# Performance work log

Measured on AMD Instinct MI355X. Metric: run time of the kernel, lower is better.

## Reference

```python
import jax, jax.numpy as jnp
import numpy as np

B, L, W, K, G = 8, 2048, 1024, 5, 2
OFFSET_SCALE = 2.0
EPS = 1e-5


def setup_inputs() -> dict:
    key = jax.random.key(0)
    ks = jax.random.split(key, 6)
    x = jax.random.normal(ks[0], (B, L, W), jnp.float32)
    # True = padded position
    lengths = jax.random.randint(ks[1], (B,), L // 2, L + 1)
    mask = jnp.arange(L)[None, :] >= lengths[:, None]
    # offset predictor (pointwise): one fractional offset per kernel tap
    w_off = jax.random.normal(ks[2], (W, K), jnp.float32) * 0.02
    b_off = jnp.zeros((K,), jnp.float32)
    # grouped conv weights: [groups, out_per_group, in_per_group, K]
    conv_w = jax.random.normal(ks[3], (G, W // G, W // G, K), jnp.float32) * 0.02
    conv_b = jnp.zeros((W,), jnp.float32)
    gamma = jnp.ones((W,), jnp.float32)
    beta = jnp.zeros((W,), jnp.float32)
    proj_w = jax.random.normal(ks[4], (W,), jnp.float32) * 0.02
    proj_b = jnp.zeros((), jnp.float32)
    return dict(x=x, mask=mask, w_off=w_off, b_off=b_off, conv_w=conv_w,
                conv_b=conv_b, gamma=gamma, beta=beta, proj_w=proj_w, proj_b=proj_b)


def _deform_conv1d(x, w_off, b_off, conv_w, conv_b):
    # x: [B, L, W]; returns [B, L, W]
    Bb, Ll, Ww = x.shape
    Gg, Co, Ci, Kk = conv_w.shape
    # per-position, per-tap fractional offsets in [-offset_scale, offset_scale]
    offsets = jnp.tanh(x @ w_off + b_off) * OFFSET_SCALE            # [B, L, K]
    taps = jnp.arange(Kk, dtype=x.dtype) - (Kk - 1) / 2.0           # centered taps
    pos = jnp.arange(Ll, dtype=x.dtype)[None, :, None] + taps[None, None, :] + offsets  # [B,L,K]
    p0 = jnp.floor(pos)
    frac = pos - p0                                                  # [B, L, K]
    p0i = p0.astype(jnp.int32)
    bidx = jnp.arange(Bb)[:, None, None]

    def gather(idx):
        valid = (idx >= 0) & (idx < Ll)                              # zero padding outside
        samp = x[bidx, jnp.clip(idx, 0, Ll - 1)]                     # [B, L, K, W]
        return samp * valid[..., None].astype(x.dtype)

    # linear interpolation between floor and floor+1 samples
    samp = gather(p0i) * (1.0 - frac)[..., None] + gather(p0i + 1) * frac[..., None]
    samp = samp.reshape(Bb, Ll, Kk, Gg, Ci)                          # split channels into groups
    out = jnp.einsum('blkgc,gock->blgo', samp, conv_w).reshape(Bb, Ll, Gg * Co)
    return out + conv_b


def reference(x, mask, w_off, b_off, conv_w, conv_b, gamma, beta, proj_w, proj_b):
    h = _deform_conv1d(x, w_off, b_off, conv_w, conv_b)              # [B, L, W]
    # LayerNorm over width
    mu = jnp.mean(h, axis=-1, keepdims=True)
    var = jnp.mean((h - mu) ** 2, axis=-1, keepdims=True)
    h = (h - mu) * jax.lax.rsqrt(var + EPS) * gamma + beta
    # dropout is identity in eval mode
    h = jnp.where(mask[..., None], 0.0, h)                           # masked fill
    lengths = jnp.maximum(jnp.sum(~mask, axis=1, keepdims=True).astype(h.dtype), 1.0)
    pooled = jnp.sum(h, axis=1) / lengths                            # [B, W]
    return pooled @ proj_w + proj_b                                  # [B]
```

## Files before the change

### kernel.cpp

```cpp
#include <hip/hip_runtime.h>
#include <hip/hip_bf16.h>

constexpr int Bb = 8, Ll = 2048, Ww = 1024;
constexpr int BL = Bb * Ll;

typedef short bf16x8 __attribute__((ext_vector_type(8)));
typedef float f32x4  __attribute__((ext_vector_type(4)));

__device__ inline unsigned short f2bf(float f) {
    union { float f; unsigned u; } v; v.f = f;
    unsigned u = v.u;
    unsigned r = (u + 0x7fffu + ((u >> 16) & 1u)) >> 16;
    return (unsigned short)r;
}
__device__ inline float bf2f(unsigned short h) {
    union { unsigned u; float f; } v; v.u = ((unsigned)h) << 16;
    return v.f;
}
__device__ inline unsigned lerp_pair(unsigned pa, unsigned pb, float w0, float w1) {
    union { unsigned u; float f; } alo, ahi, blo, bhi;
    alo.u = pa << 16;  ahi.u = pa & 0xffff0000u;
    blo.u = pb << 16;  bhi.u = pb & 0xffff0000u;
    float hlo = w0 * alo.f + w1 * blo.f;
    float hhi = w0 * ahi.f + w1 * bhi.f;
    union { __hip_bfloat162 h2; unsigned u; } r;
    r.h2 = __float22bfloat162_rn(float2{hlo, hhi});
    return r.u;
}

__device__ inline void gl_lds16(const unsigned short* g, unsigned short* l) {
    __builtin_amdgcn_global_load_lds(
        (const __attribute__((address_space(1))) unsigned int*)g,
        (__attribute__((address_space(3))) unsigned int*)l, 16, 0, 0);
}

__global__ void maskA_kernel(const void* __restrict__ mraw, int* __restrict__ flags) {
    const unsigned char* mb = (const unsigned char*)mraw;
    const unsigned* mw = (const unsigned*)mraw;
    int gid = blockIdx.x * 256 + threadIdx.x;
    int nonint = 0, notf = 0, hasf = 0;
    for (int i = gid; i < BL; i += 4096) { if ((i & 3) && mb[i]) nonint = 1; }
    for (int i = gid; i < BL / 4; i += 4096) {
        unsigned w = mw[i];
        if (w == 0x3f800000u) hasf = 1; else if (w) notf = 1;
    }
    if (__builtin_amdgcn_readfirstlane(__ballot(nonint) ? 1 : 0)) { if ((threadIdx.x & 63) == 0 && __ballot(nonint)) atomicOr(&flags[0], 1); }
    if ((threadIdx.x & 63) == 0) {
    }
    if (nonint) atomicOr(&flags[0], 1);
    if (notf)   atomicOr(&flags[1], 1);
    if (hasf)   atomicOr(&flags[2], 1);
}
__global__ void maskB_kernel(const void* __restrict__ mraw, const int* __restrict__ flags,
                             float* __restrict__ maskf) {
    const unsigned char* mb = (const unsigned char*)mraw;
    const unsigned* mw = (const unsigned*)mraw;
    int gid = blockIdx.x * 256 + threadIdx.x;
    int is_f32  = (!flags[1]) && flags[2];
    int is_bool = (!is_f32) && flags[0];
    for (int i = gid; i < BL; i += 4096) {
        int masked = is_bool ? (mb[i] != 0) : (mw[i] != 0u);
        maskf[i] = masked ? 0.0f : 1.0f;
    }
}

__global__ void wconv_kernel(const float* __restrict__ conv_w, unsigned short* __restrict__ w_t) {
    int gnt = blockIdx.x >> 2;
    int part = blockIdx.x & 3;
    int g = gnt / 20, nt = gnt % 20;
    int k = nt >> 2, o0 = (nt & 3) * 128;
    int tid = threadIdx.x;
    #pragma unroll
    for (int it = 0; it < 8; it++) {
        int chunk = part * 2048 + it * 256 + tid;
        int r = chunk >> 6;
        int cq = chunk & 63;
        int cs = cq >> 2, q = cq & 3;
        int o = o0 + r;
        int c0 = cs * 32 + q * 8;
        const float* src = conv_w + (((size_t)(g * 512 + o) * 512 + c0) * 5 + k);
        ushort4 lo, hi;
        lo.x = f2bf(src[0]);  lo.y = f2bf(src[5]);  lo.z = f2bf(src[10]); lo.w = f2bf(src[15]);
        hi.x = f2bf(src[20]); hi.y = f2bf(src[25]); hi.z = f2bf(src[30]); hi.w = f2bf(src[35]);
        int dst16 = (gnt * 16 + cs) * 512 + r * 4 + (q ^ (r & 3));
        *(ushort4*)&w_t[(size_t)dst16 * 8]     = lo;
        *(ushort4*)&w_t[(size_t)dst16 * 8 + 4] = hi;
    }
}

__global__ __launch_bounds__(256) void offsets_kernel(
    const float* __restrict__ x, const float* __restrict__ w_off, const float* __restrict__ b_off,
    unsigned short* __restrict__ x_bf, float4* __restrict__ pk)
{
    const int wave = threadIdx.x >> 6, lane = threadIdx.x & 63;
    const int bl = blockIdx.x * 4 + wave;
    const int l = bl & (Ll - 1);
    const int c0 = lane * 16;

    const float* xr = x + (size_t)bl * Ww + c0;
    float4 v0 = *(const float4*)(xr + 0);
    float4 v1 = *(const float4*)(xr + 4);
    float4 v2 = *(const float4*)(xr + 8);
    float4 v3 = *(const float4*)(xr + 12);
    float xv[16] = { v0.x,v0.y,v0.z,v0.w, v1.x,v1.y,v1.z,v1.w,
                     v2.x,v2.y,v2.z,v2.w, v3.x,v3.y,v3.z,v3.w };

    uint4 pa, pb;
    unsigned* pu = (unsigned*)&pa;
    #pragma unroll
    for (int j = 0; j < 4; j++) pu[j] = (unsigned)f2bf(xv[j*2]) | ((unsigned)f2bf(xv[j*2+1]) << 16);
    pu = (unsigned*)&pb;
    #pragma unroll
    for (int j = 0; j < 4; j++) pu[j] = (unsigned)f2bf(xv[8+j*2]) | ((unsigned)f2bf(xv[8+j*2+1]) << 16);
    *(uint4*)&x_bf[(size_t)bl * Ww + c0]     = pa;
    *(uint4*)&x_bf[(size_t)bl * Ww + c0 + 8] = pb;

    float acc[5] = {0.f, 0.f, 0.f, 0.f, 0.f};
    const float* wp = w_off + (size_t)c0 * 5;
    #pragma unroll
    for (int j = 0; j < 16; j++) {
        #pragma unroll
        for (int k = 0; k < 5; k++) acc[k] += xv[j] * wp[j * 5 + k];
    }
    #pragma unroll
    for (int k = 0; k < 5; k++)
        #pragma unroll
        for (int off = 32; off; off >>= 1) acc[k] += __shfl_xor(acc[k], off);

    if (lane < 5) {
        float s = (lane == 0) ? acc[0] : (lane == 1) ? acc[1] : (lane == 2) ? acc[2]
                : (lane == 3) ? acc[3] : acc[4];
        s += b_off[lane];
        float offv = tanhf(s) * 2.0f;
        float pos = (float)l + (float)(lane - 2) + offv;
        float p0 = floorf(pos);
        float frac = pos - p0;
        int i0 = (int)p0;
        int i1 = i0 + 1;
        int ok0 = (i0 >= 0) && (i0 < Ll);
        int ok1 = (i1 >= 0) && (i1 < Ll);
        float4 pkv;
        pkv.x = __int_as_float(min(max(i0, 0), Ll - 1));
        pkv.y = __int_as_float(min(max(i1, 0), Ll - 1));
        pkv.z = ok0 ? (1.0f - frac) : 0.0f;
        pkv.w = ok1 ? frac : 0.0f;
        pk[bl * 5 + lane] = pkv;
    }
}

__global__ __launch_bounds__(256, 2) void gemm_kernel(
    const unsigned short* __restrict__ x_bf, const unsigned short* __restrict__ w_t,
    const float4* __restrict__ pk, const float* __restrict__ conv_b,
    unsigned short* __restrict__ h)
{
    __shared__ unsigned short Bs[2][2 * 4096];
    const int tid = threadIdx.x;
    const int mt = blockIdx.x;
    const int nhalf = blockIdx.y;
    const int g = blockIdx.z;
    const int b = mt >> 4;
    const int lane = tid & 63, wave = tid >> 6;
    const int wr = (wave >> 1) * 64;
    const int imgsel = wave & 1;
    const int l15 = lane & 15, l4 = lane >> 4;
    const int sw = (l4 ^ (l15 & 3)) * 8;

    {
        const int nt0 = nhalf * 2;
        const unsigned short* W0 = w_t + ((size_t)((g * 20 + nt0) * 16 + 0)) * 4096;
        const unsigned short* W1 = w_t + ((size_t)((g * 20 + nt0 + 1) * 16 + 0)) * 4096;
        gl_lds16(W0 + tid * 8,        &Bs[0][tid * 8]);
        gl_lds16(W0 + 2048 + tid * 8, &Bs[0][2048 + tid * 8]);
        gl_lds16(W1 + tid * 8,        &Bs[0][4096 + tid * 8]);
        gl_lds16(W1 + 2048 + tid * 8, &Bs[0][4096 + 2048 + tid * 8]);
    }
    __syncthreads();

    f32x4 acc[4][8];
    #pragma unroll
    for (int i = 0; i < 4; i++)
        #pragma unroll
        for (int j = 0; j < 8; j++) acc[i][j] = (f32x4){0.f, 0.f, 0.f, 0.f};

    int buf = 0;
    for (int k = 0; k < 5; ++k) {
        unsigned off0[4], off1[4];
        float w0r[4], w1r[4];
        #pragma unroll
        for (int i = 0; i < 4; i++) {
            const int bl = mt * 128 + wr + i * 16 + l15;
            float4 pkv = pk[bl * 5 + k];
            const int i0 = __float_as_int(pkv.x), i1 = __float_as_int(pkv.y);
            off0[i] = (unsigned)(((b << 11) + i0) * Ww + g * 512);
            off1[i] = (unsigned)(((b << 11) + i1) * Ww + g * 512);
            w0r[i] = pkv.z; w1r[i] = pkv.w;
        }
        for (int cs = 0; cs < 16; ++cs) {
            const int it = k * 16 + cs;
            if (it < 79) {
                const int it2 = it + 1;
                const int k2 = it2 >> 4, cs2 = it2 & 15;
                const int nt0 = k2 * 4 + nhalf * 2;
                const unsigned short* W0 = w_t + ((size_t)((g * 20 + nt0) * 16 + cs2)) * 4096;
                const unsigned short* W1 = w_t + ((size_t)((g * 20 + nt0 + 1) * 16 + cs2)) * 4096;
                gl_lds16(W0 + tid * 8,        &Bs[buf ^ 1][tid * 8]);
                gl_lds16(W0 + 2048 + tid * 8, &Bs[buf ^ 1][2048 + tid * 8]);
                gl_lds16(W1 + tid * 8,        &Bs[buf ^ 1][4096 + tid * 8]);
                gl_lds16(W1 + 2048 + tid * 8, &Bs[buf ^ 1][4096 + 2048 + tid * 8]);
            }
            const int ch0 = cs * 32 + l4 * 8;
            bf16x8 af[4];
            #pragma unroll
            for (int i = 0; i < 4; i++) {
                const uint4 ua = *(const uint4*)(x_bf + off0[i] + ch0);
                const uint4 ub = *(const uint4*)(x_bf + off1[i] + ch0);
                union { unsigned u[4]; bf16x8 v; } fa;
                fa.u[0] = lerp_pair(ua.x, ub.x, w0r[i], w1r[i]);
                fa.u[1] = lerp_pair(ua.y, ub.y, w0r[i], w1r[i]);
                fa.u[2] = lerp_pair(ua.z, ub.z, w0r[i], w1r[i]);
                fa.u[3] = lerp_pair(ua.w, ub.w, w0r[i], w1r[i]);
                af[i] = fa.v;
            }
            bf16x8 bfr[8];
            #pragma unroll
            for (int j = 0; j < 8; j++)
                bfr[j] = *(const bf16x8*)&Bs[buf][imgsel * 4096 + (j * 16 + l15) * 32 + sw];
            #pragma unroll
            for (int i = 0; i < 4; i++)
                #pragma unroll
                for (int j = 0; j < 8; j++)
                    acc[i][j] = __builtin_amdgcn_mfma_f32_16x16x32_bf16(af[i], bfr[j], acc[i][j], 0, 0, 0);
            __syncthreads();
            buf ^= 1;
        }
    }
    #pragma unroll
    for (int j = 0; j < 8; j++) {
        const int col = g * 512 + nhalf * 256 + imgsel * 128 + j * 16 + l15;
        const float bias = conv_b[col];
        #pragma unroll
        for (int i = 0; i < 4; i++) {
            const int row0 = mt * 128 + wr + i * 16 + l4 * 4;
            #pragma unroll
            for (int rr = 0; rr < 4; rr++)
                h[(size_t)(row0 + rr) * Ww + col] = f2bf(acc[i][j][rr] + bias);
        }
    }
}

__global__ __launch_bounds__(256) void lnpool_kernel(
    const unsigned short* __restrict__ h, const float* __restrict__ gamma,
    const float* __restrict__ maskf, float* __restrict__ pooled)
{
    const int tid = threadIdx.x;
    const int wave = tid >> 6, lane = tid & 63;
    const int c0 = lane * 16;
    const int bl0 = blockIdx.x * 16 + wave * 4;
    const int b = bl0 >> 11;

    float g16[16];
    #pragma unroll
    for (int j = 0; j < 4; j++) {
        float4 gv = *(const float4*)(gamma + c0 + j * 4);
        g16[j*4+0] = gv.x; g16[j*4+1] = gv.y; g16[j*4+2] = gv.z; g16[j*4+3] = gv.w;
    }
    float pacc[16];
    #pragma unroll
    for (int j = 0; j < 16; j++) pacc[j] = 0.f;

    #pragma unroll
    for (int r = 0; r < 4; r++) {
        const int bl = bl0 + r;
        const float m = maskf[bl];
        const uint4 ha = *(const uint4*)(h + (size_t)bl * Ww + c0);
        const uint4 hb = *(const uint4*)(h + (size_t)bl * Ww + c0 + 8);
        float hf[16];
        const unsigned* pw = (const unsigned*)&ha;
        #pragma unroll
        for (int j = 0; j < 4; j++) {
            union { unsigned u; float f; } lo, hi;
            lo.u = pw[j] << 16; hi.u = pw[j] & 0xffff0000u;
            hf[j*2] = lo.f; hf[j*2+1] = hi.f;
        }
        pw = (const unsigned*)&hb;
        #pragma unroll
        for (int j = 0; j < 4; j++) {
            union { unsigned u; float f; } lo, hi;
            lo.u = pw[j] << 16; hi.u = pw[j] & 0xffff0000u;
            hf[8+j*2] = lo.f; hf[8+j*2+1] = hi.f;
        }
        float s1 = 0.f, s2 = 0.f;
        #pragma unroll
        for (int j = 0; j < 16; j++) { s1 += hf[j]; s2 += hf[j] * hf[j]; }
        #pragma unroll
        for (int off = 32; off; off >>= 1) {
            s1 += __shfl_xor(s1, off);
            s2 += __shfl_xor(s2, off);
        }
        const float mu = s1 * (1.0f / 1024.0f);
        const float var = s2 * (1.0f / 1024.0f) - mu * mu;
        const float rstd = rsqrtf(var + 1e-5f) * m;
        #pragma unroll
        for (int j = 0; j < 16; j++) pacc[j] += (hf[j] - mu) * rstd * g16[j];
    }
    __shared__ float spool[4][1024];
    #pragma unroll
    for (int j = 0; j < 4; j++)
        *(float4*)&spool[wave][c0 + j * 4] = *(float4*)&pacc[j * 4];
    __syncthreads();
    const int ch = tid * 4;
    float4 a = *(float4*)&spool[0][ch];
    float4 bq = *(float4*)&spool[1][ch];
    float4 cq = *(float4*)&spool[2][ch];
    float4 dq = *(float4*)&spool[3][ch];
    atomicAdd(&pooled[b * Ww + ch + 0], a.x + bq.x + cq.x + dq.x);
    atomicAdd(&pooled[b * Ww + ch + 1], a.y + bq.y + cq.y + dq.y);
    atomicAdd(&pooled[b * Ww + ch + 2], a.z + bq.z + cq.z + dq.z);
    atomicAdd(&pooled[b * Ww + ch + 3], a.w + bq.w + cq.w + dq.w);
}

__global__ void final_kernel(const float* __restrict__ pooled, const float* __restrict__ maskf,
                             const float* __restrict__ beta, const float* __restrict__ proj_w,
                             const float* __restrict__ proj_b, float* __restrict__ out)
{
    int b = blockIdx.x;
    int tid = threadIdx.x;
    float len = 0.f, dotP = 0.f, dotB = 0.f;
    for (int l = tid; l < Ll; l += 256) len += maskf[b * Ll + l];
    for (int c = tid; c < Ww; c += 256) {
        dotP += pooled[b * Ww + c] * proj_w[c];
        dotB += beta[c] * proj_w[c];
    }
    for (int off = 32; off; off >>= 1) {
        len += __shfl_down(len, off);
        dotP += __shfl_down(dotP, off);
        dotB += __shfl_down(dotB, off);
    }
    __shared__ float rl[4], rp[4], rb[4];
    int wave = tid >> 6, lane = tid & 63;
    if (lane == 0) { rl[wave] = len; rp[wave] = dotP; rb[wave] = dotB; }
    __syncthreads();
    if (tid == 0) {
        float Lt = rl[0] + rl[1] + rl[2] + rl[3];
        float Pt = rp[0] + rp[1] + rp[2] + rp[3];
        float Bt = rb[0] + rb[1] + rb[2] + rb[3];
        out[b] = Pt / fmaxf(Lt, 1.0f) + Bt + proj_b[0];
    }
}


extern "C" void kernel_launch(void* const* d_in, const int* in_sizes, int n_in,
                              void* d_out, int out_size, void* d_ws, size_t ws_size,
                              hipStream_t stream)
{
    const float* x      = (const float*)d_in[0];
    const void*  mask   = d_in[1];
    const float* w_off  = (const float*)d_in[2];
    const float* b_off  = (const float*)d_in[3];
    const float* conv_w = (const float*)d_in[4];
    const float* conv_b = (const float*)d_in[5];
    const float* gamma  = (const float*)d_in[6];
    const float* beta   = (const float*)d_in[7];
    const float* proj_w = (const float*)d_in[8];
    const float* proj_b = (const float*)d_in[9];
    float* out = (float*)d_out;

    char* ws = (char*)d_ws;
    float* maskf         = (float*)(ws + 0);
    float* pooled        = (float*)(ws + 65536);
    int*   flags         = (int*)(ws + 98304);
    float4* pk           = (float4*)(ws + 98320);
    unsigned short* w_t  = (unsigned short*)(ws + 1409040);
    unsigned short* x_bf = (unsigned short*)(ws + 6651920);
    unsigned short* h    = (unsigned short*)(ws + 40206352);

    hipMemsetAsync(pooled, 0, Bb * Ww * sizeof(float), stream);
    hipMemsetAsync(flags, 0, 16, stream);
    maskA_kernel<<<16, 256, 0, stream>>>(mask, flags);
    maskB_kernel<<<16, 256, 0, stream>>>(mask, flags, maskf);
    wconv_kernel<<<160, 256, 0, stream>>>(conv_w, w_t);
    offsets_kernel<<<BL / 4, 256, 0, stream>>>(x, w_off, b_off, x_bf, pk);
    gemm_kernel<<<dim3(128, 2, 2), 256, 0, stream>>>(x_bf, w_t, pk, conv_b, h);
    lnpool_kernel<<<1024, 256, 0, stream>>>(h, gamma, maskf, pooled);
    final_kernel<<<8, 256, 0, stream>>>(pooled, maskf, beta, proj_w, proj_b, out);
}
```

Before: 352.2 us.

## Stage interpolated A tile in shared memory and coalesce weight conversion

The GEMM now builds the interpolated A tile once per block into a double-buffered shared-memory array, alongside the weight prefetch. Before, each wave regathered and lerped its own rows from global memory, so rows were duplicated across the two waves sharing them. The weight conversion kernel is restructured so each thread reads 40 contiguous floats with vector loads and writes all five taps, replacing strided scalar reads. The change adds 16 KB of LDS per block and puts gather latency on the prefetch path, which could affect occupancy.

```diff
diff --git a/kernel.cpp b/kernel.cpp
--- a/kernel.cpp
+++ b/kernel.cpp
@@ -12,10 +12,6 @@
     unsigned u = v.u;
     unsigned r = (u + 0x7fffu + ((u >> 16) & 1u)) >> 16;
     return (unsigned short)r;
-}
-__device__ inline float bf2f(unsigned short h) {
-    union { unsigned u; float f; } v; v.u = ((unsigned)h) << 16;
-    return v.f;
 }
 __device__ inline unsigned lerp_pair(unsigned pa, unsigned pb, float w0, float w1) {
     union { unsigned u; float f; } alo, ahi, blo, bhi;
@@ -43,9 +39,6 @@
     for (int i = gid; i < BL / 4; i += 4096) {
         unsigned w = mw[i];
         if (w == 0x3f800000u) hasf = 1; else if (w) notf = 1;
-    }
-    if (__builtin_amdgcn_readfirstlane(__ballot(nonint) ? 1 : 0)) { if ((threadIdx.x & 63) == 0 && __ballot(nonint)) atomicOr(&flags[0], 1); }
-    if ((threadIdx.x & 63) == 0) {
     }
     if (nonint) atomicOr(&flags[0], 1);
     if (notf)   atomicOr(&flags[1], 1);
@@ -64,25 +57,26 @@
     }
 }
 
-__global__ void wconv_kernel(const float* __restrict__ conv_w, unsigned short* __restrict__ w_t) {
-    int gnt = blockIdx.x >> 2;
-    int part = blockIdx.x & 3;
-    int g = gnt / 20, nt = gnt % 20;
-    int k = nt >> 2, o0 = (nt & 3) * 128;
-    int tid = threadIdx.x;
-    #pragma unroll
-    for (int it = 0; it < 8; it++) {
-        int chunk = part * 2048 + it * 256 + tid;
-        int r = chunk >> 6;
-        int cq = chunk & 63;
-        int cs = cq >> 2, q = cq & 3;
-        int o = o0 + r;
-        int c0 = cs * 32 + q * 8;
-        const float* src = conv_w + (((size_t)(g * 512 + o) * 512 + c0) * 5 + k);
+__global__ __launch_bounds__(256) void wconv_kernel(const float* __restrict__ conv_w,
+                                                    unsigned short* __restrict__ w_t) {
+    int t = blockIdx.x * 256 + threadIdx.x;
+    int oct = t & 63;
+    int o   = (t >> 6) & 511;
+    int g   = t >> 15;
+    const float* src = conv_w + ((size_t)(g * 512 + o) * 512 + oct * 8) * 5;
+    float f[40];
+    #pragma unroll
+    for (int j = 0; j < 10; j++) *(float4*)&f[j * 4] = *(const float4*)&src[j * 4];
+    int r = o & 127, ob = o >> 7, cs = oct >> 2, q = oct & 3;
+    int base16 = ((g * 20 + ob) * 16 + cs) * 512 + r * 4 + (q ^ (r & 3));
+    #pragma unroll
+    for (int k = 0; k < 5; k++) {
         ushort4 lo, hi;
-        lo.x = f2bf(src[0]);  lo.y = f2bf(src[5]);  lo.z = f2bf(src[10]); lo.w = f2bf(src[15]);
-        hi.x = f2bf(src[20]); hi.y = f2bf(src[25]); hi.z = f2bf(src[30]); hi.w = f2bf(src[35]);
-        int dst16 = (gnt * 16 + cs) * 512 + r * 4 + (q ^ (r & 3));
+        lo.x = f2bf(f[0 * 5 + k]); lo.y = f2bf(f[1 * 5 + k]);
+        lo.z = f2bf(f[2 * 5 + k]); lo.w = f2bf(f[3 * 5 + k]);
+        hi.x = f2bf(f[4 * 5 + k]); hi.y = f2bf(f[5 * 5 + k]);
+        hi.z = f2bf(f[6 * 5 + k]); hi.w = f2bf(f[7 * 5 + k]);
+        int dst16 = base16 + k * 4 * 16 * 512;
         *(ushort4*)&w_t[(size_t)dst16 * 8]     = lo;
         *(ushort4*)&w_t[(size_t)dst16 * 8 + 4] = hi;
     }
@@ -154,16 +148,54 @@
     unsigned short* __restrict__ h)
 {
     __shared__ unsigned short Bs[2][2 * 4096];
+    __shared__ unsigned short As[2][4096];
     const int tid = threadIdx.x;
     const int mt = blockIdx.x;
     const int nhalf = blockIdx.y;
     const int g = blockIdx.z;
     const int b = mt >> 4;
     const int lane = tid & 63, wave = tid >> 6;
-    const int wr = (wave >> 1) * 64;
+    const int wr4 = (wave >> 1) * 4;
     const int imgsel = wave & 1;
     const int l15 = lane & 15, l4 = lane >> 4;
     const int sw = (l4 ^ (l15 & 3)) * 8;
+
+    const int arow = ((tid >> 6) << 4) + (tid & 15);
+    const int oct8 = ((tid >> 4) & 3) * 8;
+    const int bl_a = mt * 128 + arow;
+    const int bl_b = bl_a + 64;
+    const int gbase = g * 512;
+
+    unsigned off0a, off1a, off0b, off1b;
+    float w0a, w1a, w0b, w1b;
+    auto load_meta = [&](int k2) {
+        float4 pa = pk[bl_a * 5 + k2];
+        float4 pb = pk[bl_b * 5 + k2];
+        off0a = (unsigned)(((b << 11) + __float_as_int(pa.x)) * Ww + gbase);
+        off1a = (unsigned)(((b << 11) + __float_as_int(pa.y)) * Ww + gbase);
+        w0a = pa.z; w1a = pa.w;
+        off0b = (unsigned)(((b << 11) + __float_as_int(pb.x)) * Ww + gbase);
+        off1b = (unsigned)(((b << 11) + __float_as_int(pb.y)) * Ww + gbase);
+        w0b = pb.z; w1b = pb.w;
+    };
+    auto build_A = [&](int cs2, unsigned short* dst) {
+        const int ch = cs2 * 32 + oct8;
+        uint4 ua = *(const uint4*)(x_bf + off0a + ch);
+        uint4 ub = *(const uint4*)(x_bf + off1a + ch);
+        uint4 uc = *(const uint4*)(x_bf + off0b + ch);
+        uint4 ud = *(const uint4*)(x_bf + off1b + ch);
+        uint4 ra, rb;
+        ra.x = lerp_pair(ua.x, ub.x, w0a, w1a);
+        ra.y = lerp_pair(ua.y, ub.y, w0a, w1a);
+        ra.z = lerp_pair(ua.z, ub.z, w0a, w1a);
+        ra.w = lerp_pair(ua.w, ub.w, w0a, w1a);
+        rb.x = lerp_pair(uc.x, ud.x, w0b, w1b);
+        rb.y = lerp_pair(uc.y, ud.y, w0b, w1b);
+        rb.z = lerp_pair(uc.z, ud.z, w0b, w1b);
+        rb.w = lerp_pair(uc.w, ud.w, w0b, w1b);
+        *(uint4*)&dst[tid * 8]         = ra;
+        *(uint4*)&dst[(tid + 256) * 8] = rb;
+    };
 
     {
         const int nt0 = nhalf * 2;
@@ -174,6 +206,8 @@
         gl_lds16(W1 + tid * 8,        &Bs[0][4096 + tid * 8]);
         gl_lds16(W1 + 2048 + tid * 8, &Bs[0][4096 + 2048 + tid * 8]);
     }
+    load_meta(0);
+    build_A(0, &As[0][0]);
     __syncthreads();
 
     f32x4 acc[4][8];
@@ -183,64 +217,46 @@
         for (int j = 0; j < 8; j++) acc[i][j] = (f32x4){0.f, 0.f, 0.f, 0.f};
 
     int buf = 0;
-    for (int k = 0; k < 5; ++k) {
-        unsigned off0[4], off1[4];
-        float w0r[4], w1r[4];
-        #pragma unroll
-        for (int i = 0; i < 4; i++) {
-            const int bl = mt * 128 + wr + i * 16 + l15;
-            float4 pkv = pk[bl * 5 + k];
-            const int i0 = __float_as_int(pkv.x), i1 = __float_as_int(pkv.y);
-            off0[i] = (unsigned)(((b << 11) + i0) * Ww + g * 512);
-            off1[i] = (unsigned)(((b << 11) + i1) * Ww + g * 512);
-            w0r[i] = pkv.z; w1r[i] = pkv.w;
-        }
-        for (int cs = 0; cs < 16; ++cs) {
-            const int it = k * 16 + cs;
-            if (it < 79) {
-                const int it2 = it + 1;
-                const int k2 = it2 >> 4, cs2 = it2 & 15;
-                const int nt0 = k2 * 4 + nhalf * 2;
-                const unsigned short* W0 = w_t + ((size_t)((g * 20 + nt0) * 16 + cs2)) * 4096;
-                const unsigned short* W1 = w_t + ((size_t)((g * 20 + nt0 + 1) * 16 + cs2)) * 4096;
-                gl_lds16(W0 + tid * 8,        &Bs[buf ^ 1][tid * 8]);
-                gl_lds16(W0 + 2048 + tid * 8, &Bs[buf ^ 1][2048 + tid * 8]);
-                gl_lds16(W1 + tid * 8,        &Bs[buf ^ 1][4096 + tid * 8]);
-                gl_lds16(W1 + 2048 + tid * 8, &Bs[buf ^ 1][4096 + 2048 + tid * 8]);
-            }
-            const int ch0 = cs * 32 + l4 * 8;
+    for (int it = 0; it < 80; ++it) {
+        const int it2 = it + 1;
+        if (it2 < 80) {
+            const int k2 = it2 >> 4, cs2 = it2 & 15;
+            const int nt0 = k2 * 4 + nhalf * 2;
+            const unsigned short* W0 = w_t + ((size_t)((g * 20 + nt0) * 16 + cs2)) * 4096;
+            const unsigned short* W1 = w_t + ((size_t)((g * 20 + nt0 + 1) * 16 + cs2)) * 4096;
+            unsigned short* bd = &Bs[buf ^ 1][0];
+            gl_lds16(W0 + tid * 8,        bd + tid * 8);
+            gl_lds16(W0 + 2048 + tid * 8, bd + 2048 + tid * 8);
+            gl_lds16(W1 + tid * 8,        bd + 4096 + tid * 8);
+            gl_lds16(W1 + 2048 + tid * 8, bd + 4096 + 2048 + tid * 8);
+            if (cs2 == 0) load_meta(k2);
+            build_A(cs2, &As[buf ^ 1][0]);
+        }
+        {
             bf16x8 af[4];
             #pragma unroll
-            for (int i = 0; i < 4; i++) {
-                const uint4 ua = *(const uint4*)(x_bf + off0[i] + ch0);
-                const uint4 ub = *(const uint4*)(x_bf + off1[i] + ch0);
-                union { unsigned u[4]; bf16x8 v; } fa;
-                fa.u[0] = lerp_pair(ua.x, ub.x, w0r[i], w1r[i]);
-                fa.u[1] = lerp_pair(ua.y, ub.y, w0r[i], w1r[i]);
-                fa.u[2] = lerp_pair(ua.z, ub.z, w0r[i], w1r[i]);
-                fa.u[3] = lerp_pair(ua.w, ub.w, w0r[i], w1r[i]);
-                af[i] = fa.v;
+            for (int i = 0; i < 4; i++)
+                af[i] = *(const bf16x8*)&As[buf][((wr4 + i) * 64 + lane) * 8];
+            const unsigned short* bsrc = &Bs[buf][imgsel * 4096];
+            #pragma unroll
+            for (int j = 0; j < 8; j++) {
+                bf16x8 bj = *(const bf16x8*)&bsrc[(j * 16 + l15) * 32 + sw];
+                #pragma unroll
+                for (int i = 0; i < 4; i++)
+                    acc[i][j] = __builtin_amdgcn_mfma_f32_16x16x32_bf16(af[i], bj, acc[i][j], 0, 0, 0);
             }
-            bf16x8 bfr[8];
-            #pragma unroll
-            for (int j = 0; j < 8; j++)
-                bfr[j] = *(const bf16x8*)&Bs[buf][imgsel * 4096 + (j * 16 + l15) * 32 + sw];
-            #pragma unroll
-            for (int i = 0; i < 4; i++)
-                #pragma unroll
-                for (int j = 0; j < 8; j++)
-                    acc[i][j] = __builtin_amdgcn_mfma_f32_16x16x32_bf16(af[i], bfr[j], acc[i][j], 0, 0, 0);
-            __syncthreads();
-            buf ^= 1;
-        }
-    }
+        }
+        __syncthreads();
+        buf ^= 1;
+    }
+
     #pragma unroll
     for (int j = 0; j < 8; j++) {
         const int col = g * 512 + nhalf * 256 + imgsel * 128 + j * 16 + l15;
         const float bias = conv_b[col];
         #pragma unroll
         for (int i = 0; i < 4; i++) {
-            const int row0 = mt * 128 + wr + i * 16 + l4 * 4;
+            const int row0 = mt * 128 + (wave >> 1) * 64 + i * 16 + l4 * 4;
             #pragma unroll
             for (int rr = 0; rr < 4; rr++)
                 h[(size_t)(row0 + rr) * Ww + col] = f2bf(acc[i][j][rr] + bias);
@@ -378,7 +394,7 @@
     hipMemsetAsync(flags, 0, 16, stream);
     maskA_kernel<<<16, 256, 0, stream>>>(mask, flags);
     maskB_kernel<<<16, 256, 0, stream>>>(mask, flags, maskf);
-    wconv_kernel<<<160, 256, 0, stream>>>(conv_w, w_t);
+    wconv_kernel<<<256, 256, 0, stream>>>(conv_w, w_t);
     offsets_kernel<<<BL / 4, 256, 0, stream>>>(x, w_off, b_off, x_bf, pk);
     gemm_kernel<<<dim3(128, 2, 2), 256, 0, stream>>>(x_bf, w_t, pk, conv_b, h);
     lnpool_kernel<<<1024, 256, 0, stream>>>(h, gamma, maskf, pooled);
```

After: 321.0 us. 1.1x faster.
